# Performance work log

Hardware: AMD Instinct MI355X
Metric: run time of the kernel (lower is better)

## Reference

```python
import jax, jax.numpy as jnp
import numpy as np

N = 100000
E = 1200000
D = 64  # in_dim == out_dim


def leaky_relu(x, slope=0.2):
    return jnp.where(x >= 0, x, slope * x)


def setup_inputs() -> dict:
    key = jax.random.key(0)
    ks = jax.random.split(key, 10)
    indices = jax.random.randint(ks[0], (2, E), 0, N, dtype=jnp.int64)
    features = jax.random.normal(ks[1], (N, D), dtype=jnp.float32)
    e_r = jax.random.normal(ks[2], (E, D), dtype=jnp.float32)
    s = 1.0 / np.sqrt(D)
    W1_w = jax.random.normal(ks[3], (D, D), dtype=jnp.float32) * s
    W1_b = jax.random.normal(ks[4], (D,), dtype=jnp.float32) * s
    W2_w = jax.random.normal(ks[5], (D, D), dtype=jnp.float32) * s
    W2_b = jax.random.normal(ks[6], (D,), dtype=jnp.float32) * s
    Watt_w = jax.random.normal(ks[7], (D, D), dtype=jnp.float32) * s
    Watt_b = jax.random.normal(ks[8], (D,), dtype=jnp.float32) * s
    return {"indices": indices, "features": features, "e_r": e_r, "num_nodes": N,
            "W1_w": W1_w, "W1_b": W1_b, "W2_w": W2_w, "W2_b": W2_b,
            "Watt_w": Watt_w, "Watt_b": Watt_b}


def reference(indices, features, e_r, num_nodes, W1_w, W1_b, W2_w, W2_b, Watt_w, Watt_b):
    src, dst = indices[0], indices[1]
    out_dim = Watt_w.shape[0]

    # edge attention scores
    h_trans = features @ Watt_w.T + Watt_b          # (N, D)
    h_src = h_trans[src]                            # (E, D) gather
    h_dst = h_trans[dst]                            # (E, D) gather
    # e_r already aligned to out_dim (d_r == out_dim here)
    e_raw = jnp.sum(h_dst * jnp.tanh(h_src + e_r), axis=-1, keepdims=True)  # (E, 1)
    scaling = 1.0 / (out_dim ** 0.5)
    e_ij = leaky_relu(e_raw * scaling).astype(jnp.float32)

    # segment softmax over edges grouped by dst (max detached, as in original)
    max_score = jax.ops.segment_max(jax.lax.stop_gradient(e_ij), dst,
                                    num_segments=num_nodes)               # (N, 1)
    exp_e = jnp.exp(e_ij - max_score[dst])                                 # (E, 1)
    denom = jax.ops.segment_sum(exp_e, dst, num_segments=num_nodes)       # (N, 1)
    alpha = exp_e / (denom[dst] + 1e-9)                                    # (E, 1)

    # weighted scatter aggregation
    weighted_msg = features[src] * alpha.astype(features.dtype)            # (E, D)
    h_neigh = jax.ops.segment_sum(weighted_msg, dst, num_segments=num_nodes)  # (N, D)

    sum_h = features + h_neigh
    prod_h = features * h_neigh
    h_out = leaky_relu(sum_h @ W1_w.T + W1_b + (prod_h @ W2_w.T + W2_b))
    return h_out
```

## Files before the change

### kernel.cpp

```cpp
#include <hip/hip_runtime.h>
#include <hip/hip_bf16.h>

#define D 64
#define SCAN_CHUNK 2048

typedef unsigned int uint_t;
typedef unsigned short ushort_t;

__device__ __forceinline__ float fast_tanh(float x) {
    float e2 = __expf(2.0f * x);
    return 1.0f - 2.0f / (e2 + 1.0f);
}

__device__ __forceinline__ float leaky(float x) {
    return x >= 0.0f ? x : 0.2f * x;
}

__device__ __forceinline__ ushort_t f2bf(float x) {
    uint_t u = __float_as_uint(x);
    u += 0x7FFFu + ((u >> 16) & 1u);
    return (ushort_t)(u >> 16);
}
__device__ __forceinline__ uint_t pack2bf(float lo, float hi) {
    return (uint_t)f2bf(lo) | ((uint_t)f2bf(hi) << 16);
}
__device__ __forceinline__ void bf8_unpack(uint4 u, float* f) {
    f[0] = __uint_as_float(u.x << 16); f[1] = __uint_as_float(u.x & 0xFFFF0000u);
    f[2] = __uint_as_float(u.y << 16); f[3] = __uint_as_float(u.y & 0xFFFF0000u);
    f[4] = __uint_as_float(u.z << 16); f[5] = __uint_as_float(u.z & 0xFFFF0000u);
    f[6] = __uint_as_float(u.w << 16); f[7] = __uint_as_float(u.w & 0xFFFF0000u);
}

__global__ __launch_bounds__(256) void k_htrans(const float* __restrict__ feat,
                                                const float* __restrict__ W,
                                                const float* __restrict__ bias,
                                                ushort_t* __restrict__ outB, int N)
{
    __shared__ float Wt[D][D];
    __shared__ float bsh[D];
    __shared__ float fs[32][D + 1];
    const int t = threadIdx.x;
    for (int i = t; i < D * D; i += 256) { Wt[i & 63][i >> 6] = W[i]; }
    if (t < D) bsh[t] = bias[t];
    const int cg = t & 15;
    const int rp = t >> 4;
    for (int g = 0; g < 2; ++g) {
        const int base = blockIdx.x * 64 + g * 32;
        __syncthreads();
        for (int i = t; i < 32 * D; i += 256) {
            int r = i >> 6, d = i & 63;
            int n = base + r;
            fs[r][d] = (n < N) ? feat[(size_t)n * D + d] : 0.0f;
        }
        __syncthreads();
        float4 acc0 = {0, 0, 0, 0}, acc1 = {0, 0, 0, 0};
        const int r0 = rp * 2, r1 = r0 + 1;
        #pragma unroll 8
        for (int d = 0; d < D; ++d) {
            const float4 w = *reinterpret_cast<const float4*>(&Wt[d][cg * 4]);
            const float f0 = fs[r0][d], f1 = fs[r1][d];
            acc0.x += f0 * w.x; acc0.y += f0 * w.y; acc0.z += f0 * w.z; acc0.w += f0 * w.w;
            acc1.x += f1 * w.x; acc1.y += f1 * w.y; acc1.z += f1 * w.z; acc1.w += f1 * w.w;
        }
        const float4 b4 = *reinterpret_cast<const float4*>(&bsh[cg * 4]);
        const int n0 = base + r0, n1 = base + r1;
        if (n0 < N) {
            uint2 o = {pack2bf(acc0.x + b4.x, acc0.y + b4.y), pack2bf(acc0.z + b4.z, acc0.w + b4.w)};
            *reinterpret_cast<uint2*>(&outB[(size_t)n0 * D + cg * 4]) = o;
        }
        if (n1 < N) {
            uint2 o = {pack2bf(acc1.x + b4.x, acc1.y + b4.y), pack2bf(acc1.z + b4.z, acc1.w + b4.w)};
            *reinterpret_cast<uint2*>(&outB[(size_t)n1 * D + cg * 4]) = o;
        }
    }
}

__global__ __launch_bounds__(256) void k_tobf(const float* __restrict__ in,
                                              ushort_t* __restrict__ out, int n8)
{
    int i = blockIdx.x * 256 + threadIdx.x;
    if (i >= n8) return;
    const float4 a = reinterpret_cast<const float4*>(in)[2 * i];
    const float4 b = reinterpret_cast<const float4*>(in)[2 * i + 1];
    uint4 o;
    o.x = pack2bf(a.x, a.y); o.y = pack2bf(a.z, a.w);
    o.z = pack2bf(b.x, b.y); o.w = pack2bf(b.z, b.w);
    reinterpret_cast<uint4*>(out)[i] = o;
}

__global__ __launch_bounds__(256) void k_hist(const int* __restrict__ dst, int* __restrict__ cnt, int E)
{
    int e = blockIdx.x * 256 + threadIdx.x;
    if (e < E) atomicAdd(&cnt[dst[e]], 1);
}

__global__ __launch_bounds__(256) void k_scan1(int* __restrict__ offs, int* __restrict__ partials, int N)
{
    __shared__ int lds[256];
    const int t = threadIdx.x;
    const int base = blockIdx.x * SCAN_CHUNK + t * 8;
    int v[8];
    #pragma unroll
    for (int i = 0; i < 8; ++i) v[i] = (base + i < N) ? offs[base + i] : 0;
    int tot = 0;
    #pragma unroll
    for (int i = 0; i < 8; ++i) { int x = v[i]; v[i] = tot; tot += x; }
    lds[t] = tot;
    __syncthreads();
    for (int off = 1; off < 256; off <<= 1) {
        int x = 0;
        if (t >= off) x = lds[t - off];
        __syncthreads();
        lds[t] += x;
        __syncthreads();
    }
    const int texc = (t == 0) ? 0 : lds[t - 1];
    #pragma unroll
    for (int i = 0; i < 8; ++i)
        if (base + i < N) offs[base + i] = v[i] + texc;
    if (t == 255) partials[blockIdx.x] = lds[255];
}

__global__ void k_scan2(int* __restrict__ partials, int NB)
{
    if (threadIdx.x == 0 && blockIdx.x == 0) {
        int run = 0;
        for (int i = 0; i < NB; ++i) { int x = partials[i]; partials[i] = run; run += x; }
    }
}

__global__ __launch_bounds__(256) void k_scan3(int* __restrict__ offs, const int* __restrict__ partials, int N)
{
    const int add = partials[blockIdx.x];
    if (add == 0) return;
    const int base = blockIdx.x * SCAN_CHUNK + threadIdx.x * 8;
    #pragma unroll
    for (int i = 0; i < 8; ++i)
        if (base + i < N) offs[base + i] += add;
}

__global__ __launch_bounds__(256) void k_scatter(const int* __restrict__ dst,
                                                 const int* __restrict__ srcA,
                                                 int* __restrict__ offs,
                                                 int2* __restrict__ es, int E)
{
    int e = blockIdx.x * 256 + threadIdx.x;
    if (e < E) {
        int pos = atomicAdd(&offs[dst[e]], 1);
        es[pos] = make_int2(e, srcA[e]);
    }
}

__global__ __launch_bounds__(256) void k_fused(const int2* __restrict__ es,
                                               const int* __restrict__ offs,
                                               const ushort_t* __restrict__ htB,
                                               const float* __restrict__ er,
                                               const ushort_t* __restrict__ featB,
                                               float* __restrict__ hneigh, int N)
{
    const int t = threadIdx.x;
    const int lane = t & 63;
    const int n = blockIdx.x * 4 + (t >> 6);
    if (n >= N) return;
    const int sg = lane >> 3;
    const int dl = lane & 7;
    const int beg = (n == 0) ? 0 : offs[n - 1];
    const int end = offs[n];
    float hd[8];
    bf8_unpack(*reinterpret_cast<const uint4*>(htB + (size_t)n * D + dl * 8), hd);
    float acc[8] = {0, 0, 0, 0, 0, 0, 0, 0};
    float den = 0.0f;
    int p = beg + sg;
    int2 cur = make_int2(0, 0);
    if (p < end) cur = es[p];
    while (p < end) {
        const int pn = p + 8;
        int2 nxt = make_int2(0, 0);
        if (pn < end) nxt = es[pn];
        float hs[8], f[8];
        bf8_unpack(*reinterpret_cast<const uint4*>(htB + (size_t)cur.y * D + dl * 8), hs);
        bf8_unpack(*reinterpret_cast<const uint4*>(featB + (size_t)cur.y * D + dl * 8), f);
        const float4 e0 = *reinterpret_cast<const float4*>(er + (size_t)cur.x * D + dl * 8);
        const float4 e1 = *reinterpret_cast<const float4*>(er + (size_t)cur.x * D + dl * 8 + 4);
        float s = hd[0] * fast_tanh(hs[0] + e0.x)
                + hd[1] * fast_tanh(hs[1] + e0.y)
                + hd[2] * fast_tanh(hs[2] + e0.z)
                + hd[3] * fast_tanh(hs[3] + e0.w)
                + hd[4] * fast_tanh(hs[4] + e1.x)
                + hd[5] * fast_tanh(hs[5] + e1.y)
                + hd[6] * fast_tanh(hs[6] + e1.z)
                + hd[7] * fast_tanh(hs[7] + e1.w);
        s += __shfl_xor(s, 1);
        s += __shfl_xor(s, 2);
        s += __shfl_xor(s, 4);
        const float ex = __expf(leaky(s * 0.125f));
        den += ex;
        #pragma unroll
        for (int j = 0; j < 8; ++j) acc[j] += ex * f[j];
        cur = nxt;
        p = pn;
    }
    #pragma unroll
    for (int m = 8; m <= 32; m <<= 1) {
        den += __shfl_xor(den, m);
        #pragma unroll
        for (int j = 0; j < 8; ++j) acc[j] += __shfl_xor(acc[j], m);
    }
    if (sg == 0) {
        const float r = __builtin_amdgcn_rcpf(den + 1e-9f);
        float4 o0 = {acc[0] * r, acc[1] * r, acc[2] * r, acc[3] * r};
        float4 o1 = {acc[4] * r, acc[5] * r, acc[6] * r, acc[7] * r};
        *reinterpret_cast<float4*>(hneigh + (size_t)n * D + dl * 8) = o0;
        *reinterpret_cast<float4*>(hneigh + (size_t)n * D + dl * 8 + 4) = o1;
    }
}

__global__ __launch_bounds__(256) void k_out(const float* __restrict__ feat,
                                             const float* __restrict__ hneigh,
                                             const float* __restrict__ W1,
                                             const float* __restrict__ b1,
                                             const float* __restrict__ W2,
                                             const float* __restrict__ b2,
                                             float* __restrict__ out, int N)
{
    __shared__ float W1t[D][D];
    __shared__ float W2t[D][D];
    __shared__ float bsum[D];
    __shared__ float ss[32][D + 1];
    __shared__ float pp[32][D + 1];
    const int t = threadIdx.x;
    for (int i = t; i < D * D; i += 256) {
        W1t[i & 63][i >> 6] = W1[i];
        W2t[i & 63][i >> 6] = W2[i];
    }
    if (t < D) bsum[t] = b1[t] + b2[t];
    const int cg = t & 15;
    const int rp = t >> 4;
    for (int g = 0; g < 2; ++g) {
        const int base = blockIdx.x * 64 + g * 32;
        __syncthreads();
        for (int i = t; i < 32 * D; i += 256) {
            int r = i >> 6, d = i & 63;
            int n = base + r;
            float f = 0.0f, hn = 0.0f;
            if (n < N) { f = feat[(size_t)n * D + d]; hn = hneigh[(size_t)n * D + d]; }
            ss[r][d] = f + hn;
            pp[r][d] = f * hn;
        }
        __syncthreads();
        float4 a0 = {0, 0, 0, 0}, a1 = {0, 0, 0, 0};
        const int r0 = rp * 2, r1 = r0 + 1;
        #pragma unroll 4
        for (int d = 0; d < D; ++d) {
            const float4 w1 = *reinterpret_cast<const float4*>(&W1t[d][cg * 4]);
            const float4 w2 = *reinterpret_cast<const float4*>(&W2t[d][cg * 4]);
            const float s0 = ss[r0][d], p0 = pp[r0][d];
            const float s1 = ss[r1][d], p1 = pp[r1][d];
            a0.x += s0 * w1.x + p0 * w2.x; a0.y += s0 * w1.y + p0 * w2.y;
            a0.z += s0 * w1.z + p0 * w2.z; a0.w += s0 * w1.w + p0 * w2.w;
            a1.x += s1 * w1.x + p1 * w2.x; a1.y += s1 * w1.y + p1 * w2.y;
            a1.z += s1 * w1.z + p1 * w2.z; a1.w += s1 * w1.w + p1 * w2.w;
        }
        const float4 b4 = *reinterpret_cast<const float4*>(&bsum[cg * 4]);
        const int n0 = base + r0, n1 = base + r1;
        if (n0 < N) {
            float4 o = {leaky(a0.x + b4.x), leaky(a0.y + b4.y), leaky(a0.z + b4.z), leaky(a0.w + b4.w)};
            *reinterpret_cast<float4*>(&out[(size_t)n0 * D + cg * 4]) = o;
        }
        if (n1 < N) {
            float4 o = {leaky(a1.x + b4.x), leaky(a1.y + b4.y), leaky(a1.z + b4.z), leaky(a1.w + b4.w)};
            *reinterpret_cast<float4*>(&out[(size_t)n1 * D + cg * 4]) = o;
        }
    }
}

extern "C" void kernel_launch(void* const* d_in, const int* in_sizes, int n_in,
                              void* d_out, int out_size, void* d_ws, size_t ws_size,
                              hipStream_t stream) {
    const int*   idx  = (const int*)d_in[0];
    const float* feat = (const float*)d_in[1];
    const float* er   = (const float*)d_in[2];
    const float* W1   = (const float*)d_in[4];
    const float* b1   = (const float*)d_in[5];
    const float* W2   = (const float*)d_in[6];
    const float* b2   = (const float*)d_in[7];
    const float* Wa   = (const float*)d_in[8];
    const float* ba   = (const float*)d_in[9];

    const int E = in_sizes[0] / 2;
    const int N = in_sizes[1] / D;
    const int* srcI = idx;
    const int* dstI = idx + E;

    float*    hneigh   = (float*)d_ws;
    ushort_t* htB      = (ushort_t*)(hneigh + (size_t)N * D);
    ushort_t* featB    = htB + (size_t)N * D;
    int2*     es       = (int2*)(featB + (size_t)N * D);
    int*      offs     = (int*)(es + E);
    int*      partials = offs + N;

    const int NB = (N + SCAN_CHUNK - 1) / SCAN_CHUNK;

    hipMemsetAsync(offs, 0, (size_t)N * sizeof(int), stream);

    dim3 blk(256);
    k_htrans <<<dim3((N + 63) / 64), blk, 0, stream>>>(feat, Wa, ba, htB, N);
    k_tobf   <<<dim3((N * D / 8 + 255) / 256), blk, 0, stream>>>(feat, featB, N * D / 8);
    k_hist   <<<dim3((E + 255) / 256), blk, 0, stream>>>(dstI, offs, E);
    k_scan1  <<<dim3(NB), blk, 0, stream>>>(offs, partials, N);
    k_scan2  <<<dim3(1), dim3(64), 0, stream>>>(partials, NB);
    k_scan3  <<<dim3(NB), blk, 0, stream>>>(offs, partials, N);
    k_scatter<<<dim3((E + 255) / 256), blk, 0, stream>>>(dstI, srcI, offs, es, E);
    k_fused  <<<dim3((N + 3) / 4), blk, 0, stream>>>(es, offs, htB, er, featB, hneigh, N);
    k_out    <<<dim3((N + 63) / 64), blk, 0, stream>>>(feat, hneigh, W1, b1, W2, b2, (float*)d_out, N);
}
```

Before: 717.3 us.

## Split edge scoring into an edge-ordered kernel and fuse bf16 feature conversion

Edge attention scores are now computed in a separate kernel that walks edges in their original order, so the large e_r tensor is read sequentially and coalesced rather than gathered through the dst-sorted permutation. The aggregation kernel then reads only a per-edge exp score and the bf16 source features. The feature-to-bf16 conversion is folded into the h_trans kernel, reusing the tile already staged in shared memory and removing one launch plus a full read of the features. The cost is an extra kernel launch, a round-trip of E floats through global memory, and a second gather of h_trans rows per edge.

```diff
diff --git a/kernel.cpp b/kernel.cpp
--- a/kernel.cpp
+++ b/kernel.cpp
@@ -34,7 +34,8 @@
 __global__ __launch_bounds__(256) void k_htrans(const float* __restrict__ feat,
                                                 const float* __restrict__ W,
                                                 const float* __restrict__ bias,
-                                                ushort_t* __restrict__ outB, int N)
+                                                ushort_t* __restrict__ htB,
+                                                ushort_t* __restrict__ featB, int N)
 {
     __shared__ float Wt[D][D];
     __shared__ float bsh[D];
@@ -53,6 +54,14 @@
             fs[r][d] = (n < N) ? feat[(size_t)n * D + d] : 0.0f;
         }
         __syncthreads();
+        for (int i = t; i < 32 * 32; i += 256) {
+            int r = i >> 5, dp = (i & 31) * 2;
+            int n = base + r;
+            if (n < N) {
+                *reinterpret_cast<uint_t*>(&featB[(size_t)n * D + dp]) =
+                    pack2bf(fs[r][dp], fs[r][dp + 1]);
+            }
+        }
         float4 acc0 = {0, 0, 0, 0}, acc1 = {0, 0, 0, 0};
         const int r0 = rp * 2, r1 = r0 + 1;
         #pragma unroll 8
@@ -66,26 +75,13 @@
         const int n0 = base + r0, n1 = base + r1;
         if (n0 < N) {
             uint2 o = {pack2bf(acc0.x + b4.x, acc0.y + b4.y), pack2bf(acc0.z + b4.z, acc0.w + b4.w)};
-            *reinterpret_cast<uint2*>(&outB[(size_t)n0 * D + cg * 4]) = o;
+            *reinterpret_cast<uint2*>(&htB[(size_t)n0 * D + cg * 4]) = o;
         }
         if (n1 < N) {
             uint2 o = {pack2bf(acc1.x + b4.x, acc1.y + b4.y), pack2bf(acc1.z + b4.z, acc1.w + b4.w)};
-            *reinterpret_cast<uint2*>(&outB[(size_t)n1 * D + cg * 4]) = o;
-        }
-    }
-}
-
-__global__ __launch_bounds__(256) void k_tobf(const float* __restrict__ in,
-                                              ushort_t* __restrict__ out, int n8)
-{
-    int i = blockIdx.x * 256 + threadIdx.x;
-    if (i >= n8) return;
-    const float4 a = reinterpret_cast<const float4*>(in)[2 * i];
-    const float4 b = reinterpret_cast<const float4*>(in)[2 * i + 1];
-    uint4 o;
-    o.x = pack2bf(a.x, a.y); o.y = pack2bf(a.z, a.w);
-    o.z = pack2bf(b.x, b.y); o.w = pack2bf(b.z, b.w);
-    reinterpret_cast<uint4*>(out)[i] = o;
+            *reinterpret_cast<uint2*>(&htB[(size_t)n1 * D + cg * 4]) = o;
+        }
+    }
 }
 
 __global__ __launch_bounds__(256) void k_hist(const int* __restrict__ dst, int* __restrict__ cnt, int E)
@@ -151,12 +147,43 @@
     }
 }
 
-__global__ __launch_bounds__(256) void k_fused(const int2* __restrict__ es,
-                                               const int* __restrict__ offs,
-                                               const ushort_t* __restrict__ htB,
-                                               const float* __restrict__ er,
-                                               const ushort_t* __restrict__ featB,
-                                               float* __restrict__ hneigh, int N)
+__global__ __launch_bounds__(256) void k_scores(const int* __restrict__ src,
+                                                const int* __restrict__ dst,
+                                                const ushort_t* __restrict__ htB,
+                                                const float* __restrict__ er,
+                                                float* __restrict__ expe, int E)
+{
+    const int gid = blockIdx.x * 256 + threadIdx.x;
+    const int lane = gid & 63;
+    const int sg = lane >> 3;
+    const int dl = lane & 7;
+    const int e = (gid >> 6) * 8 + sg;
+    if (e >= E) return;
+    const int s = src[e], dd = dst[e];
+    float hs[8], hd[8];
+    bf8_unpack(*reinterpret_cast<const uint4*>(htB + (size_t)s * D + dl * 8), hs);
+    bf8_unpack(*reinterpret_cast<const uint4*>(htB + (size_t)dd * D + dl * 8), hd);
+    const float4 e0 = *reinterpret_cast<const float4*>(er + (size_t)e * D + dl * 8);
+    const float4 e1 = *reinterpret_cast<const float4*>(er + (size_t)e * D + dl * 8 + 4);
+    float ssum = hd[0] * fast_tanh(hs[0] + e0.x)
+               + hd[1] * fast_tanh(hs[1] + e0.y)
+               + hd[2] * fast_tanh(hs[2] + e0.z)
+               + hd[3] * fast_tanh(hs[3] + e0.w)
+               + hd[4] * fast_tanh(hs[4] + e1.x)
+               + hd[5] * fast_tanh(hs[5] + e1.y)
+               + hd[6] * fast_tanh(hs[6] + e1.z)
+               + hd[7] * fast_tanh(hs[7] + e1.w);
+    ssum += __shfl_xor(ssum, 1);
+    ssum += __shfl_xor(ssum, 2);
+    ssum += __shfl_xor(ssum, 4);
+    if (dl == 0) expe[e] = __expf(leaky(ssum * 0.125f));
+}
+
+__global__ __launch_bounds__(256) void k_agg(const int2* __restrict__ es,
+                                             const int* __restrict__ offs,
+                                             const float* __restrict__ expe,
+                                             const ushort_t* __restrict__ featB,
+                                             float* __restrict__ hneigh, int N)
 {
     const int t = threadIdx.x;
     const int lane = t & 63;
@@ -166,8 +193,6 @@
     const int dl = lane & 7;
     const int beg = (n == 0) ? 0 : offs[n - 1];
     const int end = offs[n];
-    float hd[8];
-    bf8_unpack(*reinterpret_cast<const uint4*>(htB + (size_t)n * D + dl * 8), hd);
     float acc[8] = {0, 0, 0, 0, 0, 0, 0, 0};
     float den = 0.0f;
     int p = beg + sg;
@@ -177,23 +202,9 @@
         const int pn = p + 8;
         int2 nxt = make_int2(0, 0);
         if (pn < end) nxt = es[pn];
-        float hs[8], f[8];
-        bf8_unpack(*reinterpret_cast<const uint4*>(htB + (size_t)cur.y * D + dl * 8), hs);
+        const float ex = expe[cur.x];
+        float f[8];
         bf8_unpack(*reinterpret_cast<const uint4*>(featB + (size_t)cur.y * D + dl * 8), f);
-        const float4 e0 = *reinterpret_cast<const float4*>(er + (size_t)cur.x * D + dl * 8);
-        const float4 e1 = *reinterpret_cast<const float4*>(er + (size_t)cur.x * D + dl * 8 + 4);
-        float s = hd[0] * fast_tanh(hs[0] + e0.x)
-                + hd[1] * fast_tanh(hs[1] + e0.y)
-                + hd[2] * fast_tanh(hs[2] + e0.z)
-                + hd[3] * fast_tanh(hs[3] + e0.w)
-                + hd[4] * fast_tanh(hs[4] + e1.x)
-                + hd[5] * fast_tanh(hs[5] + e1.y)
-                + hd[6] * fast_tanh(hs[6] + e1.z)
-                + hd[7] * fast_tanh(hs[7] + e1.w);
-        s += __shfl_xor(s, 1);
-        s += __shfl_xor(s, 2);
-        s += __shfl_xor(s, 4);
-        const float ex = __expf(leaky(s * 0.125f));
         den += ex;
         #pragma unroll
         for (int j = 0; j < 8; ++j) acc[j] += ex * f[j];
@@ -296,7 +307,8 @@
     ushort_t* htB      = (ushort_t*)(hneigh + (size_t)N * D);
     ushort_t* featB    = htB + (size_t)N * D;
     int2*     es       = (int2*)(featB + (size_t)N * D);
-    int*      offs     = (int*)(es + E);
+    float*    expe     = (float*)(es + E);
+    int*      offs     = (int*)(expe + E);
     int*      partials = offs + N;
 
     const int NB = (N + SCAN_CHUNK - 1) / SCAN_CHUNK;
@@ -304,13 +316,13 @@
     hipMemsetAsync(offs, 0, (size_t)N * sizeof(int), stream);
 
     dim3 blk(256);
-    k_htrans <<<dim3((N + 63) / 64), blk, 0, stream>>>(feat, Wa, ba, htB, N);
-    k_tobf   <<<dim3((N * D / 8 + 255) / 256), blk, 0, stream>>>(feat, featB, N * D / 8);
+    k_htrans <<<dim3((N + 63) / 64), blk, 0, stream>>>(feat, Wa, ba, htB, featB, N);
     k_hist   <<<dim3((E + 255) / 256), blk, 0, stream>>>(dstI, offs, E);
     k_scan1  <<<dim3(NB), blk, 0, stream>>>(offs, partials, N);
     k_scan2  <<<dim3(1), dim3(64), 0, stream>>>(partials, NB);
     k_scan3  <<<dim3(NB), blk, 0, stream>>>(offs, partials, N);
     k_scatter<<<dim3((E + 255) / 256), blk, 0, stream>>>(dstI, srcI, offs, es, E);
-    k_fused  <<<dim3((N + 3) / 4), blk, 0, stream>>>(es, offs, htB, er, featB, hneigh, N);
+    k_scores <<<dim3((E + 31) / 32), blk, 0, stream>>>(srcI, dstI, htB, er, expe, E);
+    k_agg    <<<dim3((N + 3) / 4), blk, 0, stream>>>(es, offs, expe, featB, hneigh, N);
     k_out    <<<dim3((N + 63) / 64), blk, 0, stream>>>(feat, hneigh, W1, b1, W2, b2, (float*)d_out, N);
 }
```

Result: no change. 728.0 us (+1.5%).
